# Kernel tuning notes

Measured on AMD Instinct MI355X. Metric: run time of the kernel, lower is better.

The kernel has to match this reference:

```python
import jax, jax.numpy as jnp
import numpy as np

TOKENS, IN_F, OUT_F = 8192, 4096, 4096


def setup_inputs() -> dict:
    key = jax.random.key(0)
    k1, k2 = jax.random.split(key)
    return {
        "input": jax.random.normal(k1, (TOKENS, IN_F), dtype=jnp.float32),
        "weight": jax.random.normal(k2, (OUT_F, IN_F), dtype=jnp.float32),
        "weight_scale": jnp.ones((1,), dtype=jnp.float32),
        "input_scale": jnp.ones((1,), dtype=jnp.float32),
    }


def reference(input, weight, weight_scale, input_scale):
    # BitNet-style: ternary weight quantization {-1, 0, +1} w.r.t. learned scale,
    # int8-range activation quantization, fused dequant-scaled matmul.
    ws = weight_scale[0]
    xs = input_scale[0]
    # quantize_weights: round(w / ws) clipped to ternary
    w_q = jnp.clip(jnp.round(weight / ws), -1.0, 1.0)          # [out, in], values in {-1,0,1}
    # fused_quantize_matmul: quantize activations to int8 range, matmul, dequant scale
    x_q = jnp.clip(jnp.round(input / xs), -128.0, 127.0)        # [tokens, in]
    out = jnp.einsum('ti,oi->to', x_q, w_q) * (xs * ws)         # [tokens, out]
    return out
```

## Files before the change

### kernel.cpp

```cpp
#include <hip/hip_runtime.h>
#include <stdint.h>


typedef int  int4v  __attribute__((ext_vector_type(4)));
typedef int  int16v __attribute__((ext_vector_type(16)));

typedef __attribute__((address_space(1))) void gvoid;
typedef __attribute__((address_space(3))) void lvoid;

#define M_DIM 8192
#define N_DIM 4096
#define K_DIM 4096

#define BM 256
#define BN 256
#define BK 128
#define NT (K_DIM / BK)

__global__ __launch_bounds__(256) void quant_fused(
    const float* __restrict__ x, int8_t* __restrict__ xq,
    const float* __restrict__ w, int8_t* __restrict__ wq,
    const float* __restrict__ xs_ptr, const float* __restrict__ ws_ptr,
    int nx_blocks) {
  const bool isX = ((int)blockIdx.x < nx_blocks);
  const float* __restrict__ in  = isX ? x : w;
  int8_t* __restrict__ out      = isX ? xq : wq;
  const float s  = isX ? xs_ptr[0] : ws_ptr[0];
  const float lo = isX ? -128.f : -1.f;
  const float hi = isX ?  127.f :  1.f;
  const long base = (long)(isX ? blockIdx.x : (blockIdx.x - nx_blocks)) * 2048;
#pragma unroll
  for (int p = 0; p < 2; ++p) {
    const long i = base + (long)p * 1024 + (long)threadIdx.x * 4;
    float4 v = *(const float4*)(in + i);
    float e[4] = {v.x, v.y, v.z, v.w};
    union { int8_t c[4]; int u; } u;
#pragma unroll
    for (int t = 0; t < 4; ++t) {
      float q = rintf(e[t] / s);
      q = fminf(fmaxf(q, lo), hi);
      u.c[t] = (int8_t)q;
    }
    *(int*)(out + i) = u.u;
  }
}

__global__ __launch_bounds__(512, 2) void gemm_bt(
    const int8_t* __restrict__ A,
    const int8_t* __restrict__ B,
    float* __restrict__ C,
    const float* __restrict__ ws_ptr, const float* __restrict__ xs_ptr) {
  __shared__ __attribute__((aligned(16))) char smem[131072];

  const int tid  = threadIdx.x;
  const int wid  = tid >> 6;
  const int lane = tid & 63;
  const int wr   = wid >> 2;
  const int wc   = wid & 3;
  const int r    = lane & 31;
  const int half = lane >> 5;

  const int fl  = blockIdx.y * gridDim.x + blockIdx.x;
  const int vid = (fl & 7) * 64 + (fl >> 3);
  const long m0 = (long)(vid & 31) * BM;
  const long n0 = (long)(vid >> 5) * BN;

  const int srow   = wid * 8 + (lane >> 3);
  const int schunk = ((lane & 7) ^ (lane >> 3)) * 16;
  const int8_t* gA = A + (m0 + srow) * K_DIM + schunk;
  const int8_t* gB = B + (n0 + srow) * K_DIM + schunk;
  const int ldst = wid * 1024;

  int aRow[4], bRow[2], co[4];
#pragma unroll
  for (int m = 0; m < 4; ++m) aRow[m] = (wr * 128 + m * 32 + r) * BK;
#pragma unroll
  for (int n = 0; n < 2; ++n) bRow[n] = (wc * 64 + n * 32 + r) * BK;
#pragma unroll
  for (int ks = 0; ks < 4; ++ks) co[ks] = ((ks * 2 + half) ^ (r & 7)) * 16;

#define STAGE_A(kk, q, nb)                                                         \
  __builtin_amdgcn_global_load_lds(                                                \
      (gvoid*)(gA + (long)(kk) * BK + (long)(q) * 64 * K_DIM),                     \
      (lvoid*)(smem + (nb) * 32768 + (q) * 8192 + ldst), 16, 0, 0)
#define STAGE_B(kk, q, nb)                                                         \
  __builtin_amdgcn_global_load_lds(                                                \
      (gvoid*)(gB + (long)(kk) * BK + (long)(q) * 64 * K_DIM),                     \
      (lvoid*)(smem + 65536 + (nb) * 32768 + (q) * 8192 + ldst), 16, 0, 0)

  STAGE_A(0, 0, 0); STAGE_A(0, 2, 0);
  STAGE_B(0, 0, 0); STAGE_B(0, 1, 0); STAGE_B(0, 2, 0); STAGE_B(0, 3, 0);
  STAGE_A(0, 1, 0); STAGE_A(0, 3, 0);
  asm volatile("s_waitcnt vmcnt(2)" ::: "memory");
  __builtin_amdgcn_s_barrier();

  int4v  a[2][4], b0[4], b1[4];
  int16v acc[4][2] = {};

#pragma unroll 2
  for (int t = 0; t < NT; ++t) {
    const int bi = t & 1;
    const int nb = bi ^ 1;
    const char* sAb = smem + bi * 32768;
    const char* sBb = smem + 65536 + bi * 32768;
    int kk = t + 1; if (kk >= NT) kk = NT - 1;

#pragma unroll
    for (int m = 0; m < 2; ++m)
#pragma unroll
      for (int ks = 0; ks < 4; ++ks)
        a[m][ks] = *(const int4v*)(sAb + aRow[m] + co[ks]);
#pragma unroll
    for (int ks = 0; ks < 4; ++ks)
      b0[ks] = *(const int4v*)(sBb + bRow[0] + co[ks]);
#pragma unroll
    for (int ks = 0; ks < 4; ++ks)
      b1[ks] = *(const int4v*)(sBb + bRow[1] + co[ks]);
    STAGE_A(kk, 0, nb); STAGE_A(kk, 2, nb);
    STAGE_B(kk, 0, nb); STAGE_B(kk, 1, nb); STAGE_B(kk, 2, nb); STAGE_B(kk, 3, nb);
    asm volatile("s_waitcnt vmcnt(6)" ::: "memory");
    __builtin_amdgcn_s_barrier();
    __builtin_amdgcn_s_setprio(1);
#pragma unroll
    for (int ks = 0; ks < 4; ++ks) {
      acc[0][0] = __builtin_amdgcn_mfma_i32_32x32x32_i8(a[0][ks], b0[ks], acc[0][0], 0, 0, 0);
      acc[1][0] = __builtin_amdgcn_mfma_i32_32x32x32_i8(a[1][ks], b0[ks], acc[1][0], 0, 0, 0);
      acc[0][1] = __builtin_amdgcn_mfma_i32_32x32x32_i8(a[0][ks], b1[ks], acc[0][1], 0, 0, 0);
      acc[1][1] = __builtin_amdgcn_mfma_i32_32x32x32_i8(a[1][ks], b1[ks], acc[1][1], 0, 0, 0);
    }
    __builtin_amdgcn_s_setprio(0);

#pragma unroll
    for (int m = 0; m < 2; ++m)
#pragma unroll
      for (int ks = 0; ks < 4; ++ks)
        a[m][ks] = *(const int4v*)(sAb + aRow[2 + m] + co[ks]);
    STAGE_A(kk, 1, nb); STAGE_A(kk, 3, nb);
    asm volatile("s_waitcnt lgkmcnt(0)" ::: "memory");
    asm volatile("s_waitcnt vmcnt(2)" ::: "memory");
    __builtin_amdgcn_s_barrier();
    __builtin_amdgcn_s_setprio(1);
#pragma unroll
    for (int ks = 0; ks < 4; ++ks) {
      acc[2][0] = __builtin_amdgcn_mfma_i32_32x32x32_i8(a[0][ks], b0[ks], acc[2][0], 0, 0, 0);
      acc[3][0] = __builtin_amdgcn_mfma_i32_32x32x32_i8(a[1][ks], b0[ks], acc[3][0], 0, 0, 0);
      acc[2][1] = __builtin_amdgcn_mfma_i32_32x32x32_i8(a[0][ks], b1[ks], acc[2][1], 0, 0, 0);
      acc[3][1] = __builtin_amdgcn_mfma_i32_32x32x32_i8(a[1][ks], b1[ks], acc[3][1], 0, 0, 0);
    }
    __builtin_amdgcn_s_setprio(0);
  }
  asm volatile("s_waitcnt vmcnt(0)" ::: "memory");

  const float s = ws_ptr[0] * xs_ptr[0];
#pragma unroll
  for (int m = 0; m < 4; ++m) {
#pragma unroll
    for (int n = 0; n < 2; ++n) {
      const long col = n0 + wc * 64 + n * 32 + r;
      const long rowbase = m0 + wr * 128 + m * 32 + 4 * half;
#pragma unroll
      for (int reg = 0; reg < 16; ++reg) {
        const long row = rowbase + (reg & 3) + 8 * (reg >> 2);
        C[row * N_DIM + col] = (float)acc[m][n][reg] * s;
      }
    }
  }
#undef STAGE_A
#undef STAGE_B
}

extern "C" void kernel_launch(void* const* d_in, const int* in_sizes, int n_in,
                              void* d_out, int out_size, void* d_ws, size_t ws_size,
                              hipStream_t stream) {
  const float* x  = (const float*)d_in[0];
  const float* w  = (const float*)d_in[1];
  const float* ws = (const float*)d_in[2];
  const float* xs = (const float*)d_in[3];
  float* out = (float*)d_out;

  int8_t* xq = (int8_t*)d_ws;
  int8_t* wq = (int8_t*)d_ws + (size_t)M_DIM * K_DIM;

  const int nx_blocks = (int)((long)M_DIM * K_DIM / 2048);
  const int nw_blocks = (int)((long)N_DIM * K_DIM / 2048);
  quant_fused<<<nx_blocks + nw_blocks, 256, 0, stream>>>(x, xq, w, wq, xs, ws, nx_blocks);

  dim3 grid(N_DIM / BN, M_DIM / BM);
  gemm_bt<<<grid, 512, 0, stream>>>(xq, wq, out, ws, xs);
}
```

Baseline: 386.0 us.

## Prefetch two K tiles ahead and interleave LDS fragment reads with MFMAs

Restructures the GEMM main loop so global-to-LDS staging runs two tiles ahead instead of one, with each tile loaded as a full batch of eight transfers. LDS fragment reads are split per k-substep and interleaved with MFMA instructions through register double-buffering (fa0/fa1), so the next substep's operands load while the current MFMAs run. This is meant to hide LDS and global latency behind compute. In exchange it uses more registers, adds a second barrier per iteration around the staging, and drops the s_setprio hints.

```diff
diff --git a/kernel.cpp b/kernel.cpp
--- a/kernel.cpp
+++ b/kernel.cpp
@@ -77,7 +77,7 @@
 #pragma unroll
   for (int n = 0; n < 2; ++n) bRow[n] = (wc * 64 + n * 32 + r) * BK;
 #pragma unroll
-  for (int ks = 0; ks < 4; ++ks) co[ks] = ((ks * 2 + half) ^ (r & 7)) * 16;
+  for (int q = 0; q < 4; ++q) co[q] = ((q * 2 + half) ^ (r & 7)) * 16;
 
 #define STAGE_A(kk, q, nb)                                                         \
   __builtin_amdgcn_global_load_lds(                                                \
@@ -87,67 +87,66 @@
   __builtin_amdgcn_global_load_lds(                                                \
       (gvoid*)(gB + (long)(kk) * BK + (long)(q) * 64 * K_DIM),                     \
       (lvoid*)(smem + 65536 + (nb) * 32768 + (q) * 8192 + ldst), 16, 0, 0)
+#define STAGE8(kk, nb)                                                             \
+  do {                                                                             \
+    STAGE_A(kk, 0, nb); STAGE_A(kk, 1, nb); STAGE_A(kk, 2, nb); STAGE_A(kk, 3, nb);\
+    STAGE_B(kk, 0, nb); STAGE_B(kk, 1, nb); STAGE_B(kk, 2, nb); STAGE_B(kk, 3, nb);\
+  } while (0)
 
-  STAGE_A(0, 0, 0); STAGE_A(0, 2, 0);
-  STAGE_B(0, 0, 0); STAGE_B(0, 1, 0); STAGE_B(0, 2, 0); STAGE_B(0, 3, 0);
-  STAGE_A(0, 1, 0); STAGE_A(0, 3, 0);
-  asm volatile("s_waitcnt vmcnt(2)" ::: "memory");
+#define QSTEP(FMa, FMb, RDa, RDb, rsA, rsB, q)                                     \
+  do {                                                                             \
+    RDa[0] = *(const int4v*)((rsA) + aRow[0] + co[q]);                             \
+    acc[0][0] = __builtin_amdgcn_mfma_i32_32x32x32_i8(FMa[0], FMb[0], acc[0][0], 0, 0, 0); \
+    RDa[1] = *(const int4v*)((rsA) + aRow[1] + co[q]);                             \
+    acc[0][1] = __builtin_amdgcn_mfma_i32_32x32x32_i8(FMa[0], FMb[1], acc[0][1], 0, 0, 0); \
+    RDa[2] = *(const int4v*)((rsA) + aRow[2] + co[q]);                             \
+    acc[1][0] = __builtin_amdgcn_mfma_i32_32x32x32_i8(FMa[1], FMb[0], acc[1][0], 0, 0, 0); \
+    RDa[3] = *(const int4v*)((rsA) + aRow[3] + co[q]);                             \
+    acc[1][1] = __builtin_amdgcn_mfma_i32_32x32x32_i8(FMa[1], FMb[1], acc[1][1], 0, 0, 0); \
+    RDb[0] = *(const int4v*)((rsB) + bRow[0] + co[q]);                             \
+    acc[2][0] = __builtin_amdgcn_mfma_i32_32x32x32_i8(FMa[2], FMb[0], acc[2][0], 0, 0, 0); \
+    RDb[1] = *(const int4v*)((rsB) + bRow[1] + co[q]);                             \
+    acc[2][1] = __builtin_amdgcn_mfma_i32_32x32x32_i8(FMa[2], FMb[1], acc[2][1], 0, 0, 0); \
+    acc[3][0] = __builtin_amdgcn_mfma_i32_32x32x32_i8(FMa[3], FMb[0], acc[3][0], 0, 0, 0); \
+    acc[3][1] = __builtin_amdgcn_mfma_i32_32x32x32_i8(FMa[3], FMb[1], acc[3][1], 0, 0, 0); \
+  } while (0)
+
+  STAGE8(0, 0);
+  STAGE8(1, 1);
+  asm volatile("s_waitcnt vmcnt(8)" ::: "memory");
   __builtin_amdgcn_s_barrier();
+  int4v fa0[4], fb0[2], fa1[4], fb1[2];
+  {
+    const char* sA0 = smem;
+    const char* sB0 = smem + 65536;
+#pragma unroll
+    for (int m = 0; m < 4; ++m) fa0[m] = *(const int4v*)(sA0 + aRow[m] + co[0]);
+#pragma unroll
+    for (int n = 0; n < 2; ++n) fb0[n] = *(const int4v*)(sB0 + bRow[n] + co[0]);
+  }
 
-  int4v  a[2][4], b0[4], b1[4];
   int16v acc[4][2] = {};
 
 #pragma unroll 2
   for (int t = 0; t < NT; ++t) {
     const int bi = t & 1;
-    const int nb = bi ^ 1;
-    const char* sAb = smem + bi * 32768;
-    const char* sBb = smem + 65536 + bi * 32768;
-    int kk = t + 1; if (kk >= NT) kk = NT - 1;
+    const char* sA0 = smem + bi * 32768;
+    const char* sB0 = smem + 65536 + bi * 32768;
+    const char* sA1 = smem + (bi ^ 1) * 32768;
+    const char* sB1 = smem + 65536 + (bi ^ 1) * 32768;
+    int kk = t + 2; if (kk >= NT) kk = NT - 1;
 
-#pragma unroll
-    for (int m = 0; m < 2; ++m)
-#pragma unroll
-      for (int ks = 0; ks < 4; ++ks)
-        a[m][ks] = *(const int4v*)(sAb + aRow[m] + co[ks]);
-#pragma unroll
-    for (int ks = 0; ks < 4; ++ks)
-      b0[ks] = *(const int4v*)(sBb + bRow[0] + co[ks]);
-#pragma unroll
-    for (int ks = 0; ks < 4; ++ks)
-      b1[ks] = *(const int4v*)(sBb + bRow[1] + co[ks]);
-    STAGE_A(kk, 0, nb); STAGE_A(kk, 2, nb);
-    STAGE_B(kk, 0, nb); STAGE_B(kk, 1, nb); STAGE_B(kk, 2, nb); STAGE_B(kk, 3, nb);
-    asm volatile("s_waitcnt vmcnt(6)" ::: "memory");
+    QSTEP(fa0, fb0, fa1, fb1, sA0, sB0, 1);
+    QSTEP(fa1, fb1, fa0, fb0, sA0, sB0, 2);
+    QSTEP(fa0, fb0, fa1, fb1, sA0, sB0, 3);
+
+    asm volatile("s_waitcnt lgkmcnt(0)" ::: "memory");
     __builtin_amdgcn_s_barrier();
-    __builtin_amdgcn_s_setprio(1);
-#pragma unroll
-    for (int ks = 0; ks < 4; ++ks) {
-      acc[0][0] = __builtin_amdgcn_mfma_i32_32x32x32_i8(a[0][ks], b0[ks], acc[0][0], 0, 0, 0);
-      acc[1][0] = __builtin_amdgcn_mfma_i32_32x32x32_i8(a[1][ks], b0[ks], acc[1][0], 0, 0, 0);
-      acc[0][1] = __builtin_amdgcn_mfma_i32_32x32x32_i8(a[0][ks], b1[ks], acc[0][1], 0, 0, 0);
-      acc[1][1] = __builtin_amdgcn_mfma_i32_32x32x32_i8(a[1][ks], b1[ks], acc[1][1], 0, 0, 0);
-    }
-    __builtin_amdgcn_s_setprio(0);
+    STAGE8(kk, bi);
+    asm volatile("s_waitcnt vmcnt(8)" ::: "memory");
+    __builtin_amdgcn_s_barrier();
 
-#pragma unroll
-    for (int m = 0; m < 2; ++m)
-#pragma unroll
-      for (int ks = 0; ks < 4; ++ks)
-        a[m][ks] = *(const int4v*)(sAb + aRow[2 + m] + co[ks]);
-    STAGE_A(kk, 1, nb); STAGE_A(kk, 3, nb);
-    asm volatile("s_waitcnt lgkmcnt(0)" ::: "memory");
-    asm volatile("s_waitcnt vmcnt(2)" ::: "memory");
-    __builtin_amdgcn_s_barrier();
-    __builtin_amdgcn_s_setprio(1);
-#pragma unroll
-    for (int ks = 0; ks < 4; ++ks) {
-      acc[2][0] = __builtin_amdgcn_mfma_i32_32x32x32_i8(a[0][ks], b0[ks], acc[2][0], 0, 0, 0);
-      acc[3][0] = __builtin_amdgcn_mfma_i32_32x32x32_i8(a[1][ks], b0[ks], acc[3][0], 0, 0, 0);
-      acc[2][1] = __builtin_amdgcn_mfma_i32_32x32x32_i8(a[0][ks], b1[ks], acc[2][1], 0, 0, 0);
-      acc[3][1] = __builtin_amdgcn_mfma_i32_32x32x32_i8(a[1][ks], b1[ks], acc[3][1], 0, 0, 0);
-    }
-    __builtin_amdgcn_s_setprio(0);
+    QSTEP(fa1, fb1, fa0, fb0, sA1, sB1, 0);
   }
   asm volatile("s_waitcnt vmcnt(0)" ::: "memory");
 
@@ -167,6 +166,8 @@
   }
 #undef STAGE_A
 #undef STAGE_B
+#undef STAGE8
+#undef QSTEP
 }
 
 extern "C" void kernel_launch(void* const* d_in, const int* in_sizes, int n_in,
```

Result: no change. 383.9 us (-0.6%).
